# Optimization experiments

Measured on AMD Instinct MI355X. Metric: run time of the kernel, lower is better.

The kernel has to match this reference:

```python
import jax, jax.numpy as jnp
import numpy as np

# Dims: N nodes, F input feats, H1/H2 gcn widths, M modules (= n_class)
N, F, H1, H2, M = 150000, 500, 200, 8, 8


def sign01(p):
    # MySign.forward: (p > 0).float()
    return (p > 0).astype(p.dtype)


def setup_inputs() -> dict:
    key = jax.random.key(0)
    ks = jax.random.split(key, 11)
    s = 0.05  # weight scale for numerical sanity
    return {
        "x":     jax.random.normal(ks[0], (N, F), jnp.float32),
        # frozen shared GCN body
        "W1":    jax.random.normal(ks[1], (F, H1), jnp.float32) * s,
        "b1":    jnp.zeros((H1,), jnp.float32),
        "W2":    jax.random.normal(ks[2], (H1, H2), jnp.float32) * s,
        "b2":    jnp.zeros((H2,), jnp.float32),
        # per-module sign masks (torch.randn init)
        "mask1": jax.random.normal(ks[3], (M, H1), jnp.float32),
        "mask2": jax.random.normal(ks[4], (M, H2), jnp.float32),
        # per-module heads: Linear(8,8) -> ReLU -> Linear(8,1)
        "hw1":   jax.random.normal(ks[5], (M, H2, 8), jnp.float32) * s,
        "hb1":   jnp.zeros((M, 8), jnp.float32),
        "hw2":   jax.random.normal(ks[6], (M, 8), jnp.float32) * s,
        "hb2":   jnp.zeros((M,), jnp.float32),
    }


def reference(x, W1, b1, W2, b2, mask1, mask2, hw1, hb1, hw2, hb2):
    # Shared gcn1 is identical across modules -> compute once ([N,H1])
    h1 = jax.nn.relu(x @ W1 + b1)
    m1 = sign01(mask1)              # [M,H1]
    m2 = sign01(mask2)              # [M,H2]
    # per-module: mask1 * h1, then shared gcn2, then mask2 ([M,N,H2])
    h2 = jnp.einsum('nk,mk,kc->mnc', h1, m1, W2) + b2
    z = h2 * m2[:, None, :]
    # tiny 2-layer head per module, sigmoid output ([M,N])
    hid = jax.nn.relu(jnp.einsum('mnc,mch->mnh', z, hw1) + hb1[:, None, :])
    out = jax.nn.sigmoid(jnp.einsum('mnh,mh->mn', hid, hw2) + hb2[:, None])
    return out.T                    # [N, M] == torch.cat(preds, dim=1)
```

## Files before the change

kernel.cpp:

```cpp
#include <hip/hip_runtime.h>
#include <stdint.h>

#define NN       150000
#define FF       500
#define XLIM     (NN*FF - 4)
#define NTHREADS 512
#define NSTEPS   16

#define WS0_ELEMS 131072
#define WS1_ELEMS 14336

#define A_STEP   16384
#define B_BASE   32768
#define H1S_BASE 65536
#define ZS_BASE  4096

typedef short short8 __attribute__((ext_vector_type(8)));
typedef float float4v __attribute__((ext_vector_type(4)));

__device__ __forceinline__ short f2bf(float f) {
    uint32_t u = __float_as_uint(f);
    u = (u + 0x7FFFu + ((u >> 16) & 1u)) >> 16;
    return (short)u;
}
__device__ __forceinline__ float bf2f(short s) {
    return __uint_as_float(((uint32_t)(uint16_t)s) << 16);
}

__global__ __launch_bounds__(256) void prep_kernel(
    const float* __restrict__ W1, const float* __restrict__ W2,
    const float* __restrict__ mask1, short* __restrict__ ws)
{
    int idx = blockIdx.x * 256 + threadIdx.x;
    if (idx < WS0_ELEMS) {
        int t  = idx >> 13;
        int r  = idx & 8191;
        int c  = r >> 5;
        int e  = r & 31;
        int p  = e >> 3, ee = e & 7;
        int k  = t * 32 + ((p ^ (c & 3)) << 3) + ee;
        float v = (c < 200 && k < 500) ? W1[k * 200 + c] : 0.f;
        ws[idx] = f2bf(v);
    } else if (idx < WS0_ELEMS + WS1_ELEMS) {
        int r = idx - WS0_ELEMS;
        int j = r / 224;
        int k = r - j * 224;
        int m = j >> 3, c = j & 7;
        float v = 0.f;
        if (k < 200 && mask1[m * 200 + k] > 0.f) v = W2[k * 8 + c];
        ws[idx] = f2bf(v);
    }
}

#define GL16(gp, loff) __builtin_amdgcn_global_load_lds(                         \
    (const __attribute__((address_space(1))) uint32_t*)(gp),                     \
    (__attribute__((address_space(3))) uint32_t*)(lds + (loff)), 16, 0, 0)

__global__ __launch_bounds__(NTHREADS, 2) void fused_kernel(
    const float* __restrict__ x,  const float* __restrict__ b1,
    const float* __restrict__ b2, const float* __restrict__ mask2,
    const float* __restrict__ hw1, const float* __restrict__ hb1,
    const float* __restrict__ hw2, const float* __restrict__ hb2,
    const short* __restrict__ ws, float* __restrict__ out)
{
    __shared__ __align__(16) char lds[131072];
    const int tid  = threadIdx.x;
    const int lane = tid & 63;
    const int w    = tid >> 6;
    const int l15  = lane & 15;
    const int l4   = lane >> 4;
    const int n0   = blockIdx.x * 128;
    const int wrow = w >> 1;
    const int wcol = w & 1;

    int baseA[2];
    #pragma unroll
    for (int q = 0; q < 2; ++q) {
        int r  = w * 16 + q * 8 + (lane >> 3);
        int p  = lane & 7;
        int rg = n0 + r; if (rg > NN - 1) rg = NN - 1;
        baseA[q] = rg * FF + ((p ^ (r & 7)) << 2);
    }
    const int dst0 = w * 2048;
    const int dst1 = w * 2048 + 1024;
    const short* srcB0 = ws + w * 1024 + lane * 8;
    const short* srcB1 = srcB0 + 512;

    int offA[2][2], offB[7];
    #pragma unroll
    for (int i = 0; i < 2; ++i) {
        int r = wrow * 32 + i * 16 + l15;
        #pragma unroll
        for (int j = 0; j < 2; ++j) {
            int u = 2 * l4 + j;
            offA[i][j] = r * 128 + ((u ^ (r & 7)) << 4);
        }
    }
    #pragma unroll
    for (int j = 0; j < 7; ++j) {
        int c = wcol * 112 + j * 16 + l15;
        offB[j] = c * 64 + ((l4 ^ (c & 3)) << 4);
    }

    float4v acc[2][7];
    #pragma unroll
    for (int i = 0; i < 2; ++i)
        #pragma unroll
        for (int j = 0; j < 7; ++j) acc[i][j] = (float4v)0.f;

    {
        int i0 = baseA[0]; if (i0 > XLIM) i0 = XLIM;
        int i1 = baseA[1]; if (i1 > XLIM) i1 = XLIM;
        GL16(x + i0, dst0);
        GL16(x + i1, dst1);
        GL16(srcB0, B_BASE + dst0);
        GL16(srcB1, B_BASE + dst1);
    }
    #pragma unroll
    for (int t = 0; t < NSTEPS; ++t) {
        const int sel = t & 1;
        if (t < NSTEPS - 1) {
            const int o = (sel ^ 1) * A_STEP;
            int i0 = baseA[0] + (t + 1) * 32; if (i0 > XLIM) i0 = XLIM;
            int i1 = baseA[1] + (t + 1) * 32; if (i1 > XLIM) i1 = XLIM;
            GL16(x + i0, o + dst0);
            GL16(x + i1, o + dst1);
            GL16(srcB0 + (t + 1) * 8192, B_BASE + o + dst0);
            GL16(srcB1 + (t + 1) * 8192, B_BASE + o + dst1);
            asm volatile("s_waitcnt vmcnt(4)" ::: "memory");
        } else {
            asm volatile("s_waitcnt vmcnt(0)" ::: "memory");
        }
        __builtin_amdgcn_s_barrier();
        asm volatile("" ::: "memory");

        const char* pa = lds + sel * A_STEP;
        const char* pb = lds + B_BASE + sel * A_STEP;
        float4v a00 = *(const float4v*)(pa + offA[0][0]);
        float4v a01 = *(const float4v*)(pa + offA[0][1]);
        float4v a10 = *(const float4v*)(pa + offA[1][0]);
        float4v a11 = *(const float4v*)(pa + offA[1][1]);
        short8 a0, a1;
        #pragma unroll
        for (int e = 0; e < 4; ++e) { a0[e] = f2bf(a00[e]); a0[4+e] = f2bf(a01[e]); }
        #pragma unroll
        for (int e = 0; e < 4; ++e) { a1[e] = f2bf(a10[e]); a1[4+e] = f2bf(a11[e]); }
        #pragma unroll
        for (int j = 0; j < 7; ++j) {
            short8 b = *(const short8*)(pb + offB[j]);
            acc[0][j] = __builtin_amdgcn_mfma_f32_16x16x32_bf16(a0, b, acc[0][j], 0, 0, 0);
            acc[1][j] = __builtin_amdgcn_mfma_f32_16x16x32_bf16(a1, b, acc[1][j], 0, 0, 0);
        }
        asm volatile("" ::: "memory");
        __builtin_amdgcn_s_barrier();
        asm volatile("" ::: "memory");
    }

    float* smalls = (float*)lds;
    for (int i = tid; i < 944; i += NTHREADS) {
        float v;
        if      (i < 224) v = (i < 200) ? b1[i] : 0.f;
        else if (i < 232) v = b2[i - 224];
        else if (i < 296) v = (mask2[i - 232] > 0.f) ? 1.f : 0.f;
        else if (i < 808) v = hw1[i - 296];
        else if (i < 872) v = hb1[i - 808];
        else if (i < 936) v = hw2[i - 872];
        else              v = hb2[i - 936];
        smalls[i] = v;
    }
    __syncthreads();

    #pragma unroll
    for (int j = 0; j < 7; ++j) {
        int col = (wcol * 7 + j) * 16 + l15;
        float bb = smalls[col];
        int u = col >> 3, lo = (col & 7) * 2;
        #pragma unroll
        for (int i = 0; i < 2; ++i) {
            int rowb = wrow * 32 + i * 16 + l4 * 4;
            #pragma unroll
            for (int r = 0; r < 4; ++r) {
                int row = rowb + r;
                float v = acc[i][j][r] + bb;
                v = v > 0.f ? v : 0.f;
                *(short*)(lds + H1S_BASE + row * 512 + ((u ^ (row & 7)) << 4) + lo) = f2bf(v);
            }
        }
    }

    short8 b2f[7][2];
    #pragma unroll
    for (int s = 0; s < 7; ++s)
        #pragma unroll
        for (int jj = 0; jj < 2; ++jj) {
            int j = (wcol * 2 + jj) * 16 + l15;
            b2f[s][jj] = *(const short8*)(ws + WS0_ELEMS + j * 224 + s * 32 + l4 * 8);
        }
    __syncthreads();

    float4v acc2[2][2];
    #pragma unroll
    for (int i = 0; i < 2; ++i)
        #pragma unroll
        for (int jj = 0; jj < 2; ++jj) acc2[i][jj] = (float4v)0.f;

    #pragma unroll
    for (int s = 0; s < 7; ++s) {
        short8 a2[2];
        #pragma unroll
        for (int i = 0; i < 2; ++i) {
            int row = wrow * 32 + i * 16 + l15;
            int u = s * 4 + l4;
            a2[i] = *(const short8*)(lds + H1S_BASE + row * 512 + ((u ^ (row & 7)) << 4));
        }
        #pragma unroll
        for (int i = 0; i < 2; ++i)
            #pragma unroll
            for (int jj = 0; jj < 2; ++jj)
                acc2[i][jj] = __builtin_amdgcn_mfma_f32_16x16x32_bf16(a2[i], b2f[s][jj], acc2[i][jj], 0, 0, 0);
    }

    short* zs = (short*)(lds + ZS_BASE);
    #pragma unroll
    for (int jj = 0; jj < 2; ++jj) {
        int j = (wcol * 2 + jj) * 16 + l15;
        int c = j & 7;
        float bias  = smalls[224 + c];
        float scale = smalls[232 + j];
        #pragma unroll
        for (int i = 0; i < 2; ++i) {
            int rowb = wrow * 32 + i * 16 + l4 * 4;
            #pragma unroll
            for (int r = 0; r < 4; ++r) {
                float z = (acc2[i][jj][r] + bias) * scale;
                zs[(rowb + r) * 72 + j] = f2bf(z);
            }
        }
    }
    __syncthreads();

    {
        int n  = tid >> 2;
        int m0 = (tid & 3) * 2;
        short8 za = *(const short8*)(zs + n * 72 + m0 * 8);
        short8 zb = *(const short8*)(zs + n * 72 + m0 * 8 + 8);
        float o[2];
        #pragma unroll
        for (int mm = 0; mm < 2; ++mm) {
            int m = m0 + mm;
            float hid[8];
            #pragma unroll
            for (int h = 0; h < 8; ++h) hid[h] = smalls[808 + m * 8 + h];
            #pragma unroll
            for (int c = 0; c < 8; ++c) {
                float zc = bf2f(mm == 0 ? za[c] : zb[c]);
                const float* wv = smalls + 296 + (m * 8 + c) * 8;
                #pragma unroll
                for (int h = 0; h < 8; ++h) hid[h] += zc * wv[h];
            }
            float u = smalls[936 + m];
            #pragma unroll
            for (int h = 0; h < 8; ++h) {
                float hv = hid[h] > 0.f ? hid[h] : 0.f;
                u += hv * smalls[872 + m * 8 + h];
            }
            o[mm] = 1.f / (1.f + __expf(-u));
        }
        int gn = n0 + n;
        if (gn < NN) {
            float2 ov = make_float2(o[0], o[1]);
            *(float2*)(out + (long)gn * 8 + m0) = ov;
        }
    }
}

extern "C" void kernel_launch(void* const* d_in, const int* in_sizes, int n_in,
                              void* d_out, int out_size, void* d_ws, size_t ws_size,
                              hipStream_t stream)
{
    const float* x     = (const float*)d_in[0];
    const float* W1    = (const float*)d_in[1];
    const float* b1    = (const float*)d_in[2];
    const float* W2    = (const float*)d_in[3];
    const float* b2    = (const float*)d_in[4];
    const float* mask1 = (const float*)d_in[5];
    const float* mask2 = (const float*)d_in[6];
    const float* hw1   = (const float*)d_in[7];
    const float* hb1   = (const float*)d_in[8];
    const float* hw2   = (const float*)d_in[9];
    const float* hb2   = (const float*)d_in[10];
    short* ws  = (short*)d_ws;
    float* out = (float*)d_out;

    if (ws_size < (size_t)(WS0_ELEMS + WS1_ELEMS) * sizeof(short)) return;

    int prep_blocks = (WS0_ELEMS + WS1_ELEMS + 255) / 256;
    prep_kernel<<<prep_blocks, 256, 0, stream>>>(W1, W2, mask1, ws);

    int main_blocks = (NN + 127) / 128;
    fused_kernel<<<main_blocks, NTHREADS, 0, stream>>>(
        x, b1, b2, mask2, hw1, hb1, hw2, hb2, ws, out);
}
```

Baseline: 460.4 us.

## Load GEMM operands directly into registers, drop LDS staging, shrink blocks

Replaces the LDS double-buffered global_load_lds staging of x and W1 with direct per-lane register loads and a two-slot register prefetch, which removes the per-step barriers. Blocks shrink to 256 threads and 64 rows, use far less LDS, and allow higher occupancy. The W1 workspace layout is simplified to column-major with no swizzle. The bf16 conversion now uses packed v_cvt_pk_bf16_f32, and the second GEMM is restructured so each wave handles 16 rows across all 64 output columns. The risk is that direct global loads are less coalesced, and that B fragments are re-read from global/L2 by every block instead of being shared through LDS.

```diff
diff --git a/kernel.cpp b/kernel.cpp
--- a/kernel.cpp
+++ b/kernel.cpp
@@ -1,19 +1,19 @@
 #include <hip/hip_runtime.h>
 #include <stdint.h>
 
-#define NN       150000
-#define FF       500
-#define XLIM     (NN*FF - 4)
-#define NTHREADS 512
-#define NSTEPS   16
-
-#define WS0_ELEMS 131072
+#define NN        150000
+#define FF        500
+#define XBYTES    300000000u
+#define NTHREADS  256
+#define NSTEPS    16
+#define NBLOCKS   2344
+
+#define WS0_ELEMS 114688
 #define WS1_ELEMS 14336
 
-#define A_STEP   16384
-#define B_BASE   32768
-#define H1S_BASE 65536
-#define ZS_BASE  4096
+#define SMALLS_OFF 29696
+#define ZS_OFF     33472
+#define LDS_BYTES  42688
 
 typedef short short8 __attribute__((ext_vector_type(8)));
 typedef float float4v __attribute__((ext_vector_type(4)));
@@ -25,6 +25,16 @@
 }
 __device__ __forceinline__ float bf2f(short s) {
     return __uint_as_float(((uint32_t)(uint16_t)s) << 16);
+}
+__device__ __forceinline__ short8 cvt8(float4v lo, float4v hi) {
+    int r0, r1, r2, r3;
+    asm("v_cvt_pk_bf16_f32 %0, %1, %2" : "=v"(r0) : "v"(lo[0]), "v"(lo[1]));
+    asm("v_cvt_pk_bf16_f32 %0, %1, %2" : "=v"(r1) : "v"(lo[2]), "v"(lo[3]));
+    asm("v_cvt_pk_bf16_f32 %0, %1, %2" : "=v"(r2) : "v"(hi[0]), "v"(hi[1]));
+    asm("v_cvt_pk_bf16_f32 %0, %1, %2" : "=v"(r3) : "v"(hi[2]), "v"(hi[3]));
+    union { int i[4]; short8 s; } u;
+    u.i[0] = r0; u.i[1] = r1; u.i[2] = r2; u.i[3] = r3;
+    return u.s;
 }
 
 __global__ __launch_bounds__(256) void prep_kernel(
@@ -33,12 +43,7 @@
 {
     int idx = blockIdx.x * 256 + threadIdx.x;
     if (idx < WS0_ELEMS) {
-        int t  = idx >> 13;
-        int r  = idx & 8191;
-        int c  = r >> 5;
-        int e  = r & 31;
-        int p  = e >> 3, ee = e & 7;
-        int k  = t * 32 + ((p ^ (c & 3)) << 3) + ee;
+        int c = idx >> 9, k = idx & 511;
         float v = (c < 200 && k < 500) ? W1[k * 200 + c] : 0.f;
         ws[idx] = f2bf(v);
     } else if (idx < WS0_ELEMS + WS1_ELEMS) {
@@ -52,54 +57,39 @@
     }
 }
 
-#define GL16(gp, loff) __builtin_amdgcn_global_load_lds(                         \
-    (const __attribute__((address_space(1))) uint32_t*)(gp),                     \
-    (__attribute__((address_space(3))) uint32_t*)(lds + (loff)), 16, 0, 0)
-
-__global__ __launch_bounds__(NTHREADS, 2) void fused_kernel(
+__global__ __launch_bounds__(NTHREADS, 3) void fused_kernel(
     const float* __restrict__ x,  const float* __restrict__ b1,
     const float* __restrict__ b2, const float* __restrict__ mask2,
     const float* __restrict__ hw1, const float* __restrict__ hb1,
     const float* __restrict__ hw2, const float* __restrict__ hb2,
     const short* __restrict__ ws, float* __restrict__ out)
 {
-    __shared__ __align__(16) char lds[131072];
+    __shared__ __align__(16) char lds[LDS_BYTES];
+
     const int tid  = threadIdx.x;
     const int lane = tid & 63;
     const int w    = tid >> 6;
     const int l15  = lane & 15;
     const int l4   = lane >> 4;
-    const int n0   = blockIdx.x * 128;
+    const int n0   = blockIdx.x * 64;
     const int wrow = w >> 1;
     const int wcol = w & 1;
 
-    int baseA[2];
-    #pragma unroll
-    for (int q = 0; q < 2; ++q) {
-        int r  = w * 16 + q * 8 + (lane >> 3);
-        int p  = lane & 7;
-        int rg = n0 + r; if (rg > NN - 1) rg = NN - 1;
-        baseA[q] = rg * FF + ((p ^ (r & 7)) << 2);
-    }
-    const int dst0 = w * 2048;
-    const int dst1 = w * 2048 + 1024;
-    const short* srcB0 = ws + w * 1024 + lane * 8;
-    const short* srcB1 = srcB0 + 512;
-
-    int offA[2][2], offB[7];
+    const char* xb  = (const char*)x;
+    const char* wsb = (const char*)ws;
+
+    uint32_t abase[2];
     #pragma unroll
     for (int i = 0; i < 2; ++i) {
-        int r = wrow * 32 + i * 16 + l15;
-        #pragma unroll
-        for (int j = 0; j < 2; ++j) {
-            int u = 2 * l4 + j;
-            offA[i][j] = r * 128 + ((u ^ (r & 7)) << 4);
-        }
-    }
+        int row = n0 + wrow * 32 + i * 16 + l15;
+        if (row > NN - 1) row = NN - 1;
+        abase[i] = (uint32_t)row * 2000u + (uint32_t)l4 * 32u;
+    }
+    const char* bp[7];
     #pragma unroll
     for (int j = 0; j < 7; ++j) {
-        int c = wcol * 112 + j * 16 + l15;
-        offB[j] = c * 64 + ((l4 ^ (c & 3)) << 4);
+        int col = wcol * 112 + j * 16 + l15;
+        bp[j] = wsb + (uint32_t)col * 1024u + (uint32_t)l4 * 16u;
     }
 
     float4v acc[2][7];
@@ -108,55 +98,45 @@
         #pragma unroll
         for (int j = 0; j < 7; ++j) acc[i][j] = (float4v)0.f;
 
-    {
-        int i0 = baseA[0]; if (i0 > XLIM) i0 = XLIM;
-        int i1 = baseA[1]; if (i1 > XLIM) i1 = XLIM;
-        GL16(x + i0, dst0);
-        GL16(x + i1, dst1);
-        GL16(srcB0, B_BASE + dst0);
-        GL16(srcB1, B_BASE + dst1);
-    }
+    float4v alo[2][2], ahi[2][2];
+    short8  bs[7];
+
+    auto lda = [&](int slot, int t) {
+        #pragma unroll
+        for (int i = 0; i < 2; ++i) {
+            uint32_t a0 = abase[i] + (uint32_t)(t * 128);
+            uint32_t a1 = a0 + 16u;
+            if (a0 > XBYTES - 16u) a0 = XBYTES - 16u;
+            if (a1 > XBYTES - 16u) a1 = XBYTES - 16u;
+            alo[slot][i] = *(const float4v*)(xb + a0);
+            ahi[slot][i] = *(const float4v*)(xb + a1);
+        }
+    };
+    auto ldb = [&](int t) {
+        #pragma unroll
+        for (int j = 0; j < 7; ++j)
+            bs[j] = *(const short8*)(bp[j] + t * 64);
+    };
+
+    lda(0, 0);
+    lda(1, 1);
+    ldb(0);
     #pragma unroll
     for (int t = 0; t < NSTEPS; ++t) {
-        const int sel = t & 1;
-        if (t < NSTEPS - 1) {
-            const int o = (sel ^ 1) * A_STEP;
-            int i0 = baseA[0] + (t + 1) * 32; if (i0 > XLIM) i0 = XLIM;
-            int i1 = baseA[1] + (t + 1) * 32; if (i1 > XLIM) i1 = XLIM;
-            GL16(x + i0, o + dst0);
-            GL16(x + i1, o + dst1);
-            GL16(srcB0 + (t + 1) * 8192, B_BASE + o + dst0);
-            GL16(srcB1 + (t + 1) * 8192, B_BASE + o + dst1);
-            asm volatile("s_waitcnt vmcnt(4)" ::: "memory");
-        } else {
-            asm volatile("s_waitcnt vmcnt(0)" ::: "memory");
-        }
-        __builtin_amdgcn_s_barrier();
-        asm volatile("" ::: "memory");
-
-        const char* pa = lds + sel * A_STEP;
-        const char* pb = lds + B_BASE + sel * A_STEP;
-        float4v a00 = *(const float4v*)(pa + offA[0][0]);
-        float4v a01 = *(const float4v*)(pa + offA[0][1]);
-        float4v a10 = *(const float4v*)(pa + offA[1][0]);
-        float4v a11 = *(const float4v*)(pa + offA[1][1]);
-        short8 a0, a1;
-        #pragma unroll
-        for (int e = 0; e < 4; ++e) { a0[e] = f2bf(a00[e]); a0[4+e] = f2bf(a01[e]); }
-        #pragma unroll
-        for (int e = 0; e < 4; ++e) { a1[e] = f2bf(a10[e]); a1[4+e] = f2bf(a11[e]); }
+        const int slot = t & 1;
+        short8 a0 = cvt8(alo[slot][0], ahi[slot][0]);
+        short8 a1 = cvt8(alo[slot][1], ahi[slot][1]);
         #pragma unroll
         for (int j = 0; j < 7; ++j) {
-            short8 b = *(const short8*)(pb + offB[j]);
+            short8 b = bs[j];
             acc[0][j] = __builtin_amdgcn_mfma_f32_16x16x32_bf16(a0, b, acc[0][j], 0, 0, 0);
             acc[1][j] = __builtin_amdgcn_mfma_f32_16x16x32_bf16(a1, b, acc[1][j], 0, 0, 0);
         }
-        asm volatile("" ::: "memory");
-        __builtin_amdgcn_s_barrier();
-        asm volatile("" ::: "memory");
-    }
-
-    float* smalls = (float*)lds;
+        if (t + 1 < NSTEPS) ldb(t + 1);
+        if (t + 2 < NSTEPS) lda(slot, t + 2);
+    }
+
+    float* smalls = (float*)(lds + SMALLS_OFF);
     for (int i = tid; i < 944; i += NTHREADS) {
         float v;
         if      (i < 224) v = (i < 200) ? b1[i] : 0.f;
@@ -172,69 +152,64 @@
 
     #pragma unroll
     for (int j = 0; j < 7; ++j) {
-        int col = (wcol * 7 + j) * 16 + l15;
+        int col = wcol * 112 + j * 16 + l15;
         float bb = smalls[col];
-        int u = col >> 3, lo = (col & 7) * 2;
         #pragma unroll
         for (int i = 0; i < 2; ++i) {
             int rowb = wrow * 32 + i * 16 + l4 * 4;
             #pragma unroll
             for (int r = 0; r < 4; ++r) {
-                int row = rowb + r;
                 float v = acc[i][j][r] + bb;
                 v = v > 0.f ? v : 0.f;
-                *(short*)(lds + H1S_BASE + row * 512 + ((u ^ (row & 7)) << 4) + lo) = f2bf(v);
+                *(short*)(lds + (rowb + r) * 464 + col * 2) = f2bf(v);
             }
         }
     }
-
-    short8 b2f[7][2];
-    #pragma unroll
-    for (int s = 0; s < 7; ++s)
-        #pragma unroll
-        for (int jj = 0; jj < 2; ++jj) {
-            int j = (wcol * 2 + jj) * 16 + l15;
-            b2f[s][jj] = *(const short8*)(ws + WS0_ELEMS + j * 224 + s * 32 + l4 * 8);
-        }
     __syncthreads();
 
-    float4v acc2[2][2];
-    #pragma unroll
-    for (int i = 0; i < 2; ++i)
-        #pragma unroll
-        for (int jj = 0; jj < 2; ++jj) acc2[i][jj] = (float4v)0.f;
-
+    float4v acc2[4];
+    #pragma unroll
+    for (int jf = 0; jf < 4; ++jf) acc2[jf] = (float4v)0.f;
+
+    const char* wb2 = wsb + (uint32_t)WS0_ELEMS * 2u;
+    const char* b2p[4];
+    #pragma unroll
+    for (int jf = 0; jf < 4; ++jf)
+        b2p[jf] = wb2 + (uint32_t)(jf * 16 + l15) * 448u + (uint32_t)l4 * 16u;
+
+    const char* h1base = lds + (w * 16 + l15) * 464 + l4 * 16;
+
+    short8 b2c[4];
+    #pragma unroll
+    for (int jf = 0; jf < 4; ++jf) b2c[jf] = *(const short8*)(b2p[jf]);
     #pragma unroll
     for (int s = 0; s < 7; ++s) {
-        short8 a2[2];
-        #pragma unroll
-        for (int i = 0; i < 2; ++i) {
-            int row = wrow * 32 + i * 16 + l15;
-            int u = s * 4 + l4;
-            a2[i] = *(const short8*)(lds + H1S_BASE + row * 512 + ((u ^ (row & 7)) << 4));
-        }
-        #pragma unroll
-        for (int i = 0; i < 2; ++i)
-            #pragma unroll
-            for (int jj = 0; jj < 2; ++jj)
-                acc2[i][jj] = __builtin_amdgcn_mfma_f32_16x16x32_bf16(a2[i], b2f[s][jj], acc2[i][jj], 0, 0, 0);
-    }
-
-    short* zs = (short*)(lds + ZS_BASE);
-    #pragma unroll
-    for (int jj = 0; jj < 2; ++jj) {
-        int j = (wcol * 2 + jj) * 16 + l15;
-        int c = j & 7;
-        float bias  = smalls[224 + c];
+        short8 a2 = *(const short8*)(h1base + s * 64);
+        short8 b2n[4];
+        if (s < 6) {
+            #pragma unroll
+            for (int jf = 0; jf < 4; ++jf) b2n[jf] = *(const short8*)(b2p[jf] + (s + 1) * 64);
+        }
+        #pragma unroll
+        for (int jf = 0; jf < 4; ++jf)
+            acc2[jf] = __builtin_amdgcn_mfma_f32_16x16x32_bf16(a2, b2c[jf], acc2[jf], 0, 0, 0);
+        if (s < 6) {
+            #pragma unroll
+            for (int jf = 0; jf < 4; ++jf) b2c[jf] = b2n[jf];
+        }
+    }
+
+    short* zs = (short*)(lds + ZS_OFF);
+    #pragma unroll
+    for (int jf = 0; jf < 4; ++jf) {
+        int j = jf * 16 + l15;
+        float bias  = smalls[224 + (j & 7)];
         float scale = smalls[232 + j];
-        #pragma unroll
-        for (int i = 0; i < 2; ++i) {
-            int rowb = wrow * 32 + i * 16 + l4 * 4;
-            #pragma unroll
-            for (int r = 0; r < 4; ++r) {
-                float z = (acc2[i][jj][r] + bias) * scale;
-                zs[(rowb + r) * 72 + j] = f2bf(z);
-            }
+        int rowb = w * 16 + l4 * 4;
+        #pragma unroll
+        for (int r = 0; r < 4; ++r) {
+            float z = (acc2[jf][r] + bias) * scale;
+            zs[(rowb + r) * 72 + j] = f2bf(z);
         }
     }
     __syncthreads();
@@ -297,7 +272,6 @@
     int prep_blocks = (WS0_ELEMS + WS1_ELEMS + 255) / 256;
     prep_kernel<<<prep_blocks, 256, 0, stream>>>(W1, W2, mask1, ws);
 
-    int main_blocks = (NN + 127) / 128;
-    fused_kernel<<<main_blocks, NTHREADS, 0, stream>>>(
+    fused_kernel<<<NBLOCKS, NTHREADS, 0, stream>>>(
         x, b1, b2, mask2, hw1, hb1, hw2, hb2, ws, out);
 }
```

Result: slower. 564.1 us (+22.5%).
